# Optimization experiments

Hardware: AMD Instinct MI355X
Metric: run time of the kernel (lower is better)

The kernel has to match this reference:

```python
import jax, jax.numpy as jnp
import numpy as np

N_NODES = 100000
NEG_SLOPE = 0.2


def gat_conv(x, edge_index, W, a_src, a_dst, bias):
    """PyG GATConv, heads=1, concat, add_self_loops=True."""
    N = x.shape[0]
    loop = jnp.arange(N, dtype=edge_index.dtype)
    src = jnp.concatenate([edge_index[0], loop])  # message sources j
    dst = jnp.concatenate([edge_index[1], loop])  # message targets i
    h = x @ W                                      # [N, out]
    asrc = h @ a_src                               # [N]
    adst = h @ a_dst                               # [N]
    e = jax.nn.leaky_relu(asrc[src] + adst[dst], NEG_SLOPE)   # [E+N]
    m = jax.ops.segment_max(e, dst, num_segments=N)           # per-dst max
    w = jnp.exp(e - jax.lax.stop_gradient(m)[dst])
    denom = jax.ops.segment_sum(w, dst, num_segments=N)
    alpha = w / denom[dst]                                     # softmax per dst
    out = jax.ops.segment_sum(alpha[:, None] * h[src], dst, num_segments=N)
    return out + bias


def setup_inputs() -> dict:
    key = jax.random.key(0)
    ks = jax.random.split(key, 16)
    N, E, D = N_NODES, 3200000, 128
    x = jax.random.normal(ks[0], (N, D), dtype=jnp.float32)
    edge_index = jax.random.randint(ks[1], (2, E), 0, N, dtype=jnp.int64)
    def glorot(k, shape):
        fan = sum(shape)
        return jax.random.uniform(k, shape, jnp.float32, -1.0, 1.0) * np.sqrt(6.0 / fan)
    return {
        "x": x,
        "edge_index": edge_index,
        "W1": glorot(ks[2], (D, 16)),
        "a1_src": glorot(ks[3], (16,)),
        "a1_dst": glorot(ks[4], (16,)),
        "b1": jnp.zeros((16,), jnp.float32),
        "W2": glorot(ks[5], (16, 10)),
        "a2_src": glorot(ks[6], (10,)),
        "a2_dst": glorot(ks[7], (10,)),
        "b2": jnp.zeros((10,), jnp.float32),
        "Wl1": glorot(ks[8], (10, 10)),
        "bl1": jnp.zeros((10,), jnp.float32),
        "Wl2": glorot(ks[9], (10, 1)),
        "bl2": jnp.zeros((1,), jnp.float32),
    }


def reference(x, edge_index, W1, a1_src, a1_dst, b1, W2, a2_src, a2_dst, b2,
              Wl1, bl1, Wl2, bl2):
    h = gat_conv(x, edge_index, W1, a1_src, a1_dst, b1)
    h = jax.nn.relu(h)
    h = gat_conv(h, edge_index, W2, a2_src, a2_dst, b2)
    h = h @ Wl1 + bl1
    h = jax.nn.relu(h)
    return h @ Wl2 + bl2  # [N, 1]
```

## Files before the change

kernel.cpp:

```cpp
#include <hip/hip_runtime.h>
#include <hip/hip_fp16.h>


#define NEG 0.2f
#define FSH 8
#define BNODES 256
#define NSBMAX 512
#define CAP 9216
#define TILE 8192
#define PES 18

__device__ __forceinline__ float lrelu(float x) { return x > 0.0f ? x : NEG * x; }

__device__ __forceinline__ unsigned fenc(float f) {
    unsigned u = __float_as_uint(f);
    return (u & 0x80000000u) ? ~u : (u | 0x80000000u);
}
__device__ __forceinline__ float fdec(unsigned e) {
    return (e & 0x80000000u) ? __uint_as_float(e & 0x7FFFFFFFu) : __uint_as_float(~e);
}

__device__ __forceinline__ float4 ldh4(const __half* h, size_t off) {
    uint2 u = *(const uint2*)(h + off);
    __half2 a = *(__half2*)&u.x, b = *(__half2*)&u.y;
    float2 fa = __half22float2(a), fb = __half22float2(b);
    return make_float4(fa.x, fa.y, fb.x, fb.y);
}

__global__ __launch_bounds__(256) void k_init(unsigned* g, int* chist, int NSB) {
    int i = blockIdx.x * 256 + threadIdx.x;
    if (i < NSB) chist[i] = 0;
    if (i < 2) g[i] = 0u;
}

__global__ __launch_bounds__(256) void k_gemm1(
    const float* __restrict__ x, const float* __restrict__ W1,
    const float* __restrict__ a1s, const float* __restrict__ a1d,
    __half* __restrict__ h1, float* __restrict__ s1, float* __restrict__ d1,
    unsigned* __restrict__ gmax, int N)
{
    __shared__ float sW[128 * 16];
    __shared__ float sx[64 * 132];
    __shared__ float wm[4];
    int tid = threadIdx.x;
    for (int i = tid; i < 2048; i += 256) sW[i] = W1[i];
    int node0 = blockIdx.x * 64;
    for (int i = tid; i < 64 * 32; i += 256) {
        int row = i >> 5, c4 = i & 31;
        int n = node0 + row;
        float4 v = make_float4(0.f, 0.f, 0.f, 0.f);
        if (n < N) v = ((const float4*)x)[(size_t)n * 32 + c4];
        *(float4*)&sx[row * 132 + c4 * 4] = v;
    }
    __syncthreads();

    int node = node0 + (tid >> 2);
    int grp  = tid & 3;
    const float* xr = &sx[(tid >> 2) * 132];
    float4 acc = make_float4(0.f, 0.f, 0.f, 0.f);
#pragma unroll 8
    for (int j = 0; j < 128; ++j) {
        float xv = xr[j];
        float4 w = *(const float4*)&sW[j * 16 + grp * 4];
        acc.x += xv * w.x; acc.y += xv * w.y; acc.z += xv * w.z; acc.w += xv * w.w;
    }
    float4 as = ((const float4*)a1s)[grp];
    float4 ad = ((const float4*)a1d)[grp];
    float sv = acc.x * as.x + acc.y * as.y + acc.z * as.z + acc.w * as.w;
    float dv = acc.x * ad.x + acc.y * ad.y + acc.z * ad.z + acc.w * ad.w;
    sv += __shfl_xor(sv, 1); sv += __shfl_xor(sv, 2);
    dv += __shfl_xor(dv, 1); dv += __shfl_xor(dv, 2);
    if (node < N) {
        __half2 p0 = __floats2half2_rn(acc.x, acc.y);
        __half2 p1 = __floats2half2_rn(acc.z, acc.w);
        uint2 u; u.x = *(unsigned*)&p0; u.y = *(unsigned*)&p1;
        *(uint2*)&h1[(size_t)node * 16 + grp * 4] = u;
        if (grp == 0) { s1[node] = sv; d1[node] = dv; }
    }
    float m = (node < N) ? sv : -3.4e38f;
#pragma unroll
    for (int off = 32; off >= 1; off >>= 1) m = fmaxf(m, __shfl_xor(m, off));
    if ((tid & 63) == 0) wm[tid >> 6] = m;
    __syncthreads();
    if (tid == 0) {
        float b = fmaxf(fmaxf(wm[0], wm[1]), fmaxf(wm[2], wm[3]));
        atomicMax(gmax, fenc(b));
    }
}

__global__ __launch_bounds__(256) void k_chist(const int* __restrict__ edst,
                                               int* __restrict__ chist, int E, int NSB) {
    __shared__ int lc[NSBMAX];
    int tid = threadIdx.x;
    for (int i = tid; i < NSB; i += 256) lc[i] = 0;
    __syncthreads();
    int stride = gridDim.x * 256;
    for (int e = blockIdx.x * 256 + tid; e < E; e += stride)
        atomicAdd(&lc[edst[e] >> FSH], 1);
    __syncthreads();
    for (int i = tid; i < NSB; i += 256) { int v = lc[i]; if (v) atomicAdd(&chist[i], v); }
}

__global__ __launch_bounds__(512) void k_cboffs(const int* __restrict__ chist,
                                                int* __restrict__ cboffs, int* __restrict__ ccur,
                                                int NSB, int E) {
    __shared__ int wsum[8];
    int tid = threadIdx.x;
    int c = (tid < NSB) ? chist[tid] : 0;
    int pfx = c;
#pragma unroll
    for (int off = 1; off < 64; off <<= 1) {
        int t = __shfl_up(pfx, off, 64);
        if ((tid & 63) >= off) pfx += t;
    }
    if ((tid & 63) == 63) wsum[tid >> 6] = pfx;
    __syncthreads();
    int carry = 0;
    for (int w = 0; w < (tid >> 6); ++w) carry += wsum[w];
    pfx += carry;
    if (tid < NSB) { cboffs[tid] = pfx - c; ccur[tid * 16] = pfx - c; }
    if (tid == 0) cboffs[NSB] = E;
}

__global__ __launch_bounds__(512) void k_csplit(
    const int* __restrict__ esrc, const int* __restrict__ edst,
    int* __restrict__ ccur, unsigned* __restrict__ pairs, int E, int NSB)
{
    __shared__ unsigned lsrt[TILE];
    __shared__ int lhist[NSBMAX];
    __shared__ int lofs[NSBMAX + 1];
    __shared__ int gbase[NSBMAX];
    __shared__ int wsum[8];
    int tid = threadIdx.x;
    int base = blockIdx.x * TILE;
    int tcnt = min(TILE, E - base);
    for (int i = tid; i < NSB; i += 512) lhist[i] = 0;
    __syncthreads();
    for (int i = tid; i < tcnt; i += 512)
        atomicAdd(&lhist[edst[base + i] >> FSH], 1);
    __syncthreads();
    int c = (tid < NSB) ? lhist[tid] : 0;
    int pfx = c;
#pragma unroll
    for (int off = 1; off < 64; off <<= 1) {
        int t = __shfl_up(pfx, off, 64);
        if ((tid & 63) >= off) pfx += t;
    }
    if ((tid & 63) == 63) wsum[tid >> 6] = pfx;
    __syncthreads();
    int carry = 0;
    for (int w = 0; w < (tid >> 6); ++w) carry += wsum[w];
    pfx += carry;
    if (tid < NSB) {
        lofs[tid + 1] = pfx;
        gbase[tid] = c ? atomicAdd(&ccur[tid * 16], c) : 0;
        lhist[tid] = pfx - c;
    }
    if (tid == 0) lofs[0] = 0;
    __syncthreads();
    for (int i = tid; i < tcnt; i += 512) {
        int e = base + i;
        int d = edst[e], s = esrc[e];
        int pos = atomicAdd(&lhist[d >> FSH], 1);
        lsrt[pos] = ((unsigned)(d & (BNODES - 1)) << 17) | (unsigned)s;
    }
    __syncthreads();
    for (int i = tid; i < tcnt; i += 512) {
        int lo = 0, hi = NSB - 1;
        while (lo < hi) { int mid = (lo + hi + 1) >> 1; if (lofs[mid] <= i) lo = mid; else hi = mid - 1; }
        pairs[gbase[lo] + (i - lofs[lo])] = lsrt[i];
    }
}

__global__ __launch_bounds__(512) void k_agg1(
    const int* __restrict__ boffs, const unsigned* __restrict__ pairs,
    const float* __restrict__ s1, const float* __restrict__ d1, const __half* __restrict__ h1,
    const float* __restrict__ b1, const float* __restrict__ W2,
    const float* __restrict__ a2s, const float* __restrict__ a2d,
    __half* __restrict__ h2, float* __restrict__ s2, float* __restrict__ d2,
    const unsigned* __restrict__ gmax1p, unsigned* __restrict__ gmax2, int N)
{
    __shared__ unsigned srt[CAP];
    __shared__ float accs[BNODES * 17];
    __shared__ int lcnt[BNODES];
    __shared__ int lofs[BNODES + 1];
    __shared__ float dds[BNODES], mbs[BNODES];
    __shared__ float sW[160], sb[16], sas[16], sad[16];
    __shared__ int wsum[8];
    __shared__ float wm[8];

    int tid = threadIdx.x;
    int fb = blockIdx.x;
    if (tid < 160) sW[tid] = W2[tid];
    if (tid < 16) {
        sb[tid]  = b1[tid];
        sas[tid] = (tid < 10) ? a2s[tid] : 0.f;
        sad[tid] = (tid < 10) ? a2d[tid] : 0.f;
    }
    int node0 = fb << FSH;
    float g0 = fdec(*gmax1p);
    if (tid < BNODES) {
        int n = node0 + tid;
        float dd = (n < N) ? d1[n] : 0.f;
        dds[tid] = dd; mbs[tid] = lrelu(g0 + dd);
        lcnt[tid] = 0;
    }
    __syncthreads();

    int jbeg = boffs[fb], jend = boffs[fb + 1];
    int cnt = jend - jbeg;

    unsigned pe[PES];
#pragma unroll
    for (int u = 0; u < PES; ++u) {
        int i = tid + u * 512;
        bool ok = (i < cnt);
        pe[u] = ok ? pairs[jbeg + i] : 0u;
        if (ok) atomicAdd(&lcnt[(pe[u] >> 17) & (BNODES - 1)], 1);
    }
    __syncthreads();
    int c = (tid < BNODES) ? lcnt[tid] : 0;
    int pfx = c;
#pragma unroll
    for (int off = 1; off < 64; off <<= 1) {
        int t = __shfl_up(pfx, off, 64);
        if ((tid & 63) >= off) pfx += t;
    }
    if ((tid & 63) == 63) wsum[tid >> 6] = pfx;
    __syncthreads();
    int carry = 0;
    for (int w = 0; w < (tid >> 6); ++w) carry += wsum[w];
    pfx += carry;
    if (tid < BNODES) { lofs[tid + 1] = pfx; lcnt[tid] = pfx - c; }
    if (tid == 0) lofs[0] = 0;
    __syncthreads();
    int total = lofs[BNODES];

    int gg = tid >> 2, q = tid & 3;
    float4 accv[2]; float den[2];
#pragma unroll
    for (int qq = 0; qq < 2; ++qq) {
        int nl = gg * 2 + qq, n = node0 + nl;
        if (n < N) {
            float w = __expf(lrelu(s1[n] + dds[nl]) - mbs[nl]);
            float4 hv = ldh4(h1, (size_t)n * 16 + 4 * q);
            accv[qq] = make_float4(w * hv.x, w * hv.y, w * hv.z, w * hv.w);
            den[qq] = w;
        } else { accv[qq] = make_float4(0.f, 0.f, 0.f, 0.f); den[qq] = 0.f; }
    }

    if (total <= CAP && cnt <= CAP) {
#pragma unroll
        for (int u = 0; u < PES; ++u) {
            int i = tid + u * 512;
            if (i < cnt) {
                unsigned p = pe[u];
                int pos = atomicAdd(&lcnt[(p >> 17) & (BNODES - 1)], 1);
                srt[pos] = p & 0x1FFFF;
            }
        }
        __syncthreads();
#pragma unroll
        for (int qq = 0; qq < 2; ++qq) {
            int nl = gg * 2 + qq;
            float dd = dds[nl], mb = mbs[nl];
            int j = lofs[nl], j1 = lofs[nl + 1];
            float4 a = accv[qq]; float dn = den[qq];
            for (; j + 4 <= j1; j += 4) {
                int e0 = srt[j], e1 = srt[j + 1], e2 = srt[j + 2], e3 = srt[j + 3];
                float v0 = s1[e0], v1 = s1[e1], v2 = s1[e2], v3 = s1[e3];
                float4 H0 = ldh4(h1, (size_t)e0 * 16 + 4 * q);
                float4 H1 = ldh4(h1, (size_t)e1 * 16 + 4 * q);
                float4 H2 = ldh4(h1, (size_t)e2 * 16 + 4 * q);
                float4 H3 = ldh4(h1, (size_t)e3 * 16 + 4 * q);
                float w0 = __expf(lrelu(v0 + dd) - mb), w1 = __expf(lrelu(v1 + dd) - mb);
                float w2 = __expf(lrelu(v2 + dd) - mb), w3 = __expf(lrelu(v3 + dd) - mb);
                a.x += w0 * H0.x + w1 * H1.x + w2 * H2.x + w3 * H3.x;
                a.y += w0 * H0.y + w1 * H1.y + w2 * H2.y + w3 * H3.y;
                a.z += w0 * H0.z + w1 * H1.z + w2 * H2.z + w3 * H3.z;
                a.w += w0 * H0.w + w1 * H1.w + w2 * H2.w + w3 * H3.w;
                dn += (w0 + w1) + (w2 + w3);
            }
            for (; j < j1; ++j) {
                int e0 = srt[j];
                float w0 = __expf(lrelu(s1[e0] + dd) - mb);
                float4 H0 = ldh4(h1, (size_t)e0 * 16 + 4 * q);
                a.x += w0 * H0.x; a.y += w0 * H0.y; a.z += w0 * H0.z; a.w += w0 * H0.w;
                dn += w0;
            }
            accv[qq] = a; den[qq] = dn;
        }
        __syncthreads();
    } else {
        for (int i = tid; i < BNODES * 17; i += 512) accs[i] = 0.f;
        __syncthreads();
        for (int i = tid; i < cnt; i += 512) {
            unsigned p = pairs[jbeg + i];
            int src = p & 0x1FFFF, nl = (p >> 17) & (BNODES - 1);
            float w = __expf(lrelu(s1[src] + dds[nl]) - mbs[nl]);
            float4 H = ldh4(h1, (size_t)src * 16 + 4 * q);
            atomicAdd(&accs[nl * 17 + 4 * q + 0], w * H.x);
            atomicAdd(&accs[nl * 17 + 4 * q + 1], w * H.y);
            atomicAdd(&accs[nl * 17 + 4 * q + 2], w * H.z);
            atomicAdd(&accs[nl * 17 + 4 * q + 3], w * H.w);
            if (q == 0) atomicAdd(&accs[nl * 17 + 16], w);
        }
        __syncthreads();
#pragma unroll
        for (int qq = 0; qq < 2; ++qq) {
            int nl = gg * 2 + qq;
            accv[qq].x += accs[nl * 17 + 4 * q + 0];
            accv[qq].y += accs[nl * 17 + 4 * q + 1];
            accv[qq].z += accs[nl * 17 + 4 * q + 2];
            accv[qq].w += accs[nl * 17 + 4 * q + 3];
            den[qq] += accs[nl * 17 + 16];
        }
        __syncthreads();
    }

#pragma unroll
    for (int qq = 0; qq < 2; ++qq) {
        int nl = gg * 2 + qq;
        accs[nl * 17 + 4 * q + 0] = accv[qq].x;
        accs[nl * 17 + 4 * q + 1] = accv[qq].y;
        accs[nl * 17 + 4 * q + 2] = accv[qq].z;
        accs[nl * 17 + 4 * q + 3] = accv[qq].w;
        if (q == 0) accs[nl * 17 + 16] = den[qq];
    }
    __syncthreads();

    int g = tid >> 4, k = tid & 15;
    float sval = -3.4e38f;
#pragma unroll
    for (int qq = 0; qq < 8; ++qq) {
        int nl = g * 8 + qq, n = node0 + nl;
        if (n >= N) continue;
        float inv = 1.f / accs[nl * 17 + 16];
        float o = fmaxf(accs[nl * 17 + k] * inv + sb[k], 0.f);
        float hh = 0.f;
#pragma unroll
        for (int kk = 0; kk < 16; ++kk) {
            float ov = __shfl(o, kk, 16);
            if (k < 10) hh += ov * sW[kk * 10 + k];
        }
        if (k >= 10) hh = 0.f;
        float ts = hh * sas[k];
        float td = hh * sad[k];
#pragma unroll
        for (int off = 1; off < 16; off <<= 1) {
            ts += __shfl_xor(ts, off, 16);
            td += __shfl_xor(td, off, 16);
        }
        h2[(size_t)n * 16 + k] = __float2half_rn(hh);
        if (k == 0) { s2[n] = ts; d2[n] = td; }
        sval = fmaxf(sval, ts);
    }
    float m = sval;
#pragma unroll
    for (int off = 32; off >= 1; off >>= 1) m = fmaxf(m, __shfl_xor(m, off));
    if ((tid & 63) == 0) wm[tid >> 6] = m;
    __syncthreads();
    if (tid == 0) {
        float b = wm[0];
#pragma unroll
        for (int i = 1; i < 8; ++i) b = fmaxf(b, wm[i]);
        atomicMax(gmax2, fenc(b));
    }
}

__global__ __launch_bounds__(512) void k_agg2(
    const int* __restrict__ boffs, const unsigned* __restrict__ pairs,
    const float* __restrict__ s2, const float* __restrict__ d2, const __half* __restrict__ h2,
    const float* __restrict__ b2, const float* __restrict__ Wl1, const float* __restrict__ bl1,
    const float* __restrict__ Wl2, const float* __restrict__ bl2,
    const unsigned* __restrict__ gmax2p, float* __restrict__ out, int N)
{
    __shared__ unsigned srt[CAP];
    __shared__ float accs[BNODES * 17];
    __shared__ int lcnt[BNODES];
    __shared__ int lofs[BNODES + 1];
    __shared__ float dds[BNODES], mbs[BNODES];
    __shared__ float sW1[100], sb1[16], sW2[16], sb2g[16];
    __shared__ float sbl2;
    __shared__ int wsum[8];

    int tid = threadIdx.x;
    int fb = blockIdx.x;
    if (tid < 100) sW1[tid] = Wl1[tid];
    if (tid < 16) {
        sb1[tid]  = (tid < 10) ? bl1[tid] : 0.f;
        sW2[tid]  = (tid < 10) ? Wl2[tid] : 0.f;
        sb2g[tid] = (tid < 10) ? b2[tid]  : 0.f;
    }
    if (tid == 0) sbl2 = bl2[0];
    int node0 = fb << FSH;
    float g0 = fdec(*gmax2p);
    if (tid < BNODES) {
        int n = node0 + tid;
        float dd = (n < N) ? d2[n] : 0.f;
        dds[tid] = dd; mbs[tid] = lrelu(g0 + dd);
        lcnt[tid] = 0;
    }
    __syncthreads();

    int jbeg = boffs[fb], jend = boffs[fb + 1];
    int cnt = jend - jbeg;

    unsigned pe[PES];
#pragma unroll
    for (int u = 0; u < PES; ++u) {
        int i = tid + u * 512;
        bool ok = (i < cnt);
        pe[u] = ok ? pairs[jbeg + i] : 0u;
        if (ok) atomicAdd(&lcnt[(pe[u] >> 17) & (BNODES - 1)], 1);
    }
    __syncthreads();
    int c = (tid < BNODES) ? lcnt[tid] : 0;
    int pfx = c;
#pragma unroll
    for (int off = 1; off < 64; off <<= 1) {
        int t = __shfl_up(pfx, off, 64);
        if ((tid & 63) >= off) pfx += t;
    }
    if ((tid & 63) == 63) wsum[tid >> 6] = pfx;
    __syncthreads();
    int carry = 0;
    for (int w = 0; w < (tid >> 6); ++w) carry += wsum[w];
    pfx += carry;
    if (tid < BNODES) { lofs[tid + 1] = pfx; lcnt[tid] = pfx - c; }
    if (tid == 0) lofs[0] = 0;
    __syncthreads();
    int total = lofs[BNODES];

    int gg = tid >> 2, q = tid & 3;
    float4 accv[2]; float den[2];
#pragma unroll
    for (int qq = 0; qq < 2; ++qq) {
        int nl = gg * 2 + qq, n = node0 + nl;
        if (n < N) {
            float w = __expf(lrelu(s2[n] + dds[nl]) - mbs[nl]);
            float4 hv = ldh4(h2, (size_t)n * 16 + 4 * q);
            accv[qq] = make_float4(w * hv.x, w * hv.y, w * hv.z, w * hv.w);
            den[qq] = w;
        } else { accv[qq] = make_float4(0.f, 0.f, 0.f, 0.f); den[qq] = 0.f; }
    }

    if (total <= CAP && cnt <= CAP) {
#pragma unroll
        for (int u = 0; u < PES; ++u) {
            int i = tid + u * 512;
            if (i < cnt) {
                unsigned p = pe[u];
                int pos = atomicAdd(&lcnt[(p >> 17) & (BNODES - 1)], 1);
                srt[pos] = p & 0x1FFFF;
            }
        }
        __syncthreads();
#pragma unroll
        for (int qq = 0; qq < 2; ++qq) {
            int nl = gg * 2 + qq;
            float dd = dds[nl], mb = mbs[nl];
            int j = lofs[nl], j1 = lofs[nl + 1];
            float4 a = accv[qq]; float dn = den[qq];
            for (; j + 4 <= j1; j += 4) {
                int e0 = srt[j], e1 = srt[j + 1], e2 = srt[j + 2], e3 = srt[j + 3];
                float v0 = s2[e0], v1 = s2[e1], v2 = s2[e2], v3 = s2[e3];
                float4 H0 = ldh4(h2, (size_t)e0 * 16 + 4 * q);
                float4 H1 = ldh4(h2, (size_t)e1 * 16 + 4 * q);
                float4 H2 = ldh4(h2, (size_t)e2 * 16 + 4 * q);
                float4 H3 = ldh4(h2, (size_t)e3 * 16 + 4 * q);
                float w0 = __expf(lrelu(v0 + dd) - mb), w1 = __expf(lrelu(v1 + dd) - mb);
                float w2 = __expf(lrelu(v2 + dd) - mb), w3 = __expf(lrelu(v3 + dd) - mb);
                a.x += w0 * H0.x + w1 * H1.x + w2 * H2.x + w3 * H3.x;
                a.y += w0 * H0.y + w1 * H1.y + w2 * H2.y + w3 * H3.y;
                a.z += w0 * H0.z + w1 * H1.z + w2 * H2.z + w3 * H3.z;
                a.w += w0 * H0.w + w1 * H1.w + w2 * H2.w + w3 * H3.w;
                dn += (w0 + w1) + (w2 + w3);
            }
            for (; j < j1; ++j) {
                int e0 = srt[j];
                float w0 = __expf(lrelu(s2[e0] + dd) - mb);
                float4 H0 = ldh4(h2, (size_t)e0 * 16 + 4 * q);
                a.x += w0 * H0.x; a.y += w0 * H0.y; a.z += w0 * H0.z; a.w += w0 * H0.w;
                dn += w0;
            }
            accv[qq] = a; den[qq] = dn;
        }
        __syncthreads();
    } else {
        for (int i = tid; i < BNODES * 17; i += 512) accs[i] = 0.f;
        __syncthreads();
        for (int i = tid; i < cnt; i += 512) {
            unsigned p = pairs[jbeg + i];
            int src = p & 0x1FFFF, nl = (p >> 17) & (BNODES - 1);
            float w = __expf(lrelu(s2[src] + dds[nl]) - mbs[nl]);
            float4 H = ldh4(h2, (size_t)src * 16 + 4 * q);
            atomicAdd(&accs[nl * 17 + 4 * q + 0], w * H.x);
            atomicAdd(&accs[nl * 17 + 4 * q + 1], w * H.y);
            atomicAdd(&accs[nl * 17 + 4 * q + 2], w * H.z);
            atomicAdd(&accs[nl * 17 + 4 * q + 3], w * H.w);
            if (q == 0) atomicAdd(&accs[nl * 17 + 16], w);
        }
        __syncthreads();
#pragma unroll
        for (int qq = 0; qq < 2; ++qq) {
            int nl = gg * 2 + qq;
            accv[qq].x += accs[nl * 17 + 4 * q + 0];
            accv[qq].y += accs[nl * 17 + 4 * q + 1];
            accv[qq].z += accs[nl * 17 + 4 * q + 2];
            accv[qq].w += accs[nl * 17 + 4 * q + 3];
            den[qq] += accs[nl * 17 + 16];
        }
        __syncthreads();
    }

#pragma unroll
    for (int qq = 0; qq < 2; ++qq) {
        int nl = gg * 2 + qq;
        accs[nl * 17 + 4 * q + 0] = accv[qq].x;
        accs[nl * 17 + 4 * q + 1] = accv[qq].y;
        accs[nl * 17 + 4 * q + 2] = accv[qq].z;
        accs[nl * 17 + 4 * q + 3] = accv[qq].w;
        if (q == 0) accs[nl * 17 + 16] = den[qq];
    }
    __syncthreads();

    int g = tid >> 4, k = tid & 15;
    bool fk = k < 10;
#pragma unroll
    for (int qq = 0; qq < 8; ++qq) {
        int nl = g * 8 + qq, n = node0 + nl;
        if (n >= N) continue;
        float inv = 1.f / accs[nl * 17 + 16];
        float o = fk ? accs[nl * 17 + k] * inv + sb2g[k] : 0.f;
        float v = sb1[k];
#pragma unroll
        for (int kk = 0; kk < 10; ++kk) {
            float ov = __shfl(o, kk, 16);
            if (fk) v += ov * sW1[kk * 10 + k];
        }
        float t = fmaxf(v, 0.f);
        float cc = t * sW2[k];
#pragma unroll
        for (int off = 1; off < 16; off <<= 1) cc += __shfl_xor(cc, off, 16);
        if (k == 0) out[n] = cc + sbl2;
    }
}

extern "C" void kernel_launch(void* const* d_in, const int* in_sizes, int n_in,
                              void* d_out, int out_size, void* d_ws, size_t ws_size,
                              hipStream_t stream)
{
    const float* x   = (const float*)d_in[0];
    const int*   ei  = (const int*)  d_in[1];
    const float* W1  = (const float*)d_in[2];
    const float* a1s = (const float*)d_in[3];
    const float* a1d = (const float*)d_in[4];
    const float* b1  = (const float*)d_in[5];
    const float* W2  = (const float*)d_in[6];
    const float* a2s = (const float*)d_in[7];
    const float* a2d = (const float*)d_in[8];
    const float* b2  = (const float*)d_in[9];
    const float* Wl1 = (const float*)d_in[10];
    const float* bl1 = (const float*)d_in[11];
    const float* Wl2 = (const float*)d_in[12];
    const float* bl2 = (const float*)d_in[13];

    int N = in_sizes[0] / 128;
    int E = in_sizes[1] / 2;
    const int* ei_src = ei;
    const int* ei_dst = ei + E;
    int NSB = (N + BNODES - 1) >> FSH;

    size_t Np = ((size_t)N + 3) & ~(size_t)3;
    size_t need_bytes = (16 + Np * 20) * 4 + ((size_t)NSB * 18 + 1) * 4 + (size_t)E * 4;
    if (ws_size < need_bytes) return;

    float*    ws    = (float*)d_ws;
    unsigned* gmax1 = (unsigned*)d_ws;
    unsigned* gmax2 = gmax1 + 1;
    __half* h1 = (__half*)(ws + 16);
    float* s1 = ws + 16 + Np * 8;
    float* d1 = s1 + Np;
    __half* h2 = (__half*)(d1 + Np);
    float* s2 = (float*)(h2) + Np * 8;
    float* d2 = s2 + Np;
    int* chist  = (int*)(d2 + Np);
    int* cboffs = chist + NSB;
    int* ccur   = cboffs + NSB + 1;
    unsigned* pairs = (unsigned*)(ccur + (size_t)NSB * 16);

    hipLaunchKernelGGL(k_init, dim3((NSB + 255) / 256), dim3(256), 0, stream, gmax1, chist, NSB);
    hipLaunchKernelGGL(k_gemm1, dim3((N + 63) / 64), dim3(256), 0, stream,
                       x, W1, a1s, a1d, h1, s1, d1, gmax1, N);
    hipLaunchKernelGGL(k_chist, dim3(256), dim3(256), 0, stream, ei_dst, chist, E, NSB);
    hipLaunchKernelGGL(k_cboffs, dim3(1), dim3(512), 0, stream, chist, cboffs, ccur, NSB, E);
    hipLaunchKernelGGL(k_csplit, dim3((E + TILE - 1) / TILE), dim3(512), 0, stream,
                       ei_src, ei_dst, ccur, pairs, E, NSB);
    hipLaunchKernelGGL(k_agg1, dim3(NSB), dim3(512), 0, stream,
                       cboffs, pairs, s1, d1, h1, b1, W2, a2s, a2d, h2, s2, d2,
                       gmax1, gmax2, N);
    hipLaunchKernelGGL(k_agg2, dim3(NSB), dim3(512), 0, stream,
                       cboffs, pairs, s2, d2, h2, b2, Wl1, bl1, Wl2, bl2,
                       gmax2, (float*)d_out, N);
}
```

Measured before the change: 297.0 us.

## Halve nodes per aggregation block and spread edge-weight exp across lanes

Shrinks the destination-node bucket from 256 to 128 nodes, which doubles the number of buckets and aggregation blocks and halves the per-block LDS staging buffer. Each quad of lanes now owns one node instead of two, so the per-thread loops over two nodes are removed. In the 4-edge unrolled loop each lane computes one exp weight and shares it with the others through quad shuffles, instead of every lane computing all four. The scan kernels now handle two buckets per thread to cover up to 1024 buckets, at the cost of more global-atomic bucket traffic in the split and smaller blocks.

```diff
diff --git a/kernel.cpp b/kernel.cpp
--- a/kernel.cpp
+++ b/kernel.cpp
@@ -3,12 +3,12 @@
 
 
 #define NEG 0.2f
-#define FSH 8
-#define BNODES 256
-#define NSBMAX 512
-#define CAP 9216
+#define FSH 7
+#define BNODES 128
+#define NSBMAX 1024
+#define CAP 4608
 #define TILE 8192
-#define PES 18
+#define PES 9
 
 __device__ __forceinline__ float lrelu(float x) { return x > 0.0f ? x : NEG * x; }
 
@@ -106,8 +106,10 @@
                                                 int NSB, int E) {
     __shared__ int wsum[8];
     int tid = threadIdx.x;
-    int c = (tid < NSB) ? chist[tid] : 0;
-    int pfx = c;
+    int i0 = 2 * tid, i1 = i0 + 1;
+    int a = (i0 < NSB) ? chist[i0] : 0;
+    int b = (i1 < NSB) ? chist[i1] : 0;
+    int s = a + b, pfx = s;
 #pragma unroll
     for (int off = 1; off < 64; off <<= 1) {
         int t = __shfl_up(pfx, off, 64);
@@ -117,8 +119,9 @@
     __syncthreads();
     int carry = 0;
     for (int w = 0; w < (tid >> 6); ++w) carry += wsum[w];
-    pfx += carry;
-    if (tid < NSB) { cboffs[tid] = pfx - c; ccur[tid * 16] = pfx - c; }
+    int excl = pfx + carry - s;
+    if (i0 < NSB) { cboffs[i0] = excl;     ccur[i0 * 16] = excl; }
+    if (i1 < NSB) { cboffs[i1] = excl + a; ccur[i1 * 16] = excl + a; }
     if (tid == 0) cboffs[NSB] = E;
 }
 
@@ -128,7 +131,7 @@
 {
     __shared__ unsigned lsrt[TILE];
     __shared__ int lhist[NSBMAX];
-    __shared__ int lofs[NSBMAX + 1];
+    __shared__ int lofs[NSBMAX];
     __shared__ int gbase[NSBMAX];
     __shared__ int wsum[8];
     int tid = threadIdx.x;
@@ -139,8 +142,10 @@
     for (int i = tid; i < tcnt; i += 512)
         atomicAdd(&lhist[edst[base + i] >> FSH], 1);
     __syncthreads();
-    int c = (tid < NSB) ? lhist[tid] : 0;
-    int pfx = c;
+    int i0 = 2 * tid, i1 = i0 + 1;
+    int a = (i0 < NSB) ? lhist[i0] : 0;
+    int b = (i1 < NSB) ? lhist[i1] : 0;
+    int s = a + b, pfx = s;
 #pragma unroll
     for (int off = 1; off < 64; off <<= 1) {
         int t = __shfl_up(pfx, off, 64);
@@ -150,19 +155,24 @@
     __syncthreads();
     int carry = 0;
     for (int w = 0; w < (tid >> 6); ++w) carry += wsum[w];
-    pfx += carry;
-    if (tid < NSB) {
-        lofs[tid + 1] = pfx;
-        gbase[tid] = c ? atomicAdd(&ccur[tid * 16], c) : 0;
-        lhist[tid] = pfx - c;
-    }
-    if (tid == 0) lofs[0] = 0;
+    int excl = pfx + carry - s;
+    if (i0 < NSB) {
+        lofs[i0] = excl;
+        gbase[i0] = a ? atomicAdd(&ccur[i0 * 16], a) : 0;
+    }
+    if (i1 < NSB) {
+        lofs[i1] = excl + a;
+        gbase[i1] = b ? atomicAdd(&ccur[i1 * 16], b) : 0;
+    }
+    __syncthreads();
+    if (i0 < NSB) lhist[i0] = lofs[i0];
+    if (i1 < NSB) lhist[i1] = lofs[i1];
     __syncthreads();
     for (int i = tid; i < tcnt; i += 512) {
         int e = base + i;
-        int d = edst[e], s = esrc[e];
+        int d = edst[e], srcv = esrc[e];
         int pos = atomicAdd(&lhist[d >> FSH], 1);
-        lsrt[pos] = ((unsigned)(d & (BNODES - 1)) << 17) | (unsigned)s;
+        lsrt[pos] = ((unsigned)(d & (BNODES - 1)) << 17) | (unsigned)srcv;
     }
     __syncthreads();
     for (int i = tid; i < tcnt; i += 512) {
@@ -237,17 +247,14 @@
     int total = lofs[BNODES];
 
     int gg = tid >> 2, q = tid & 3;
-    float4 accv[2]; float den[2];
-#pragma unroll
-    for (int qq = 0; qq < 2; ++qq) {
-        int nl = gg * 2 + qq, n = node0 + nl;
-        if (n < N) {
-            float w = __expf(lrelu(s1[n] + dds[nl]) - mbs[nl]);
-            float4 hv = ldh4(h1, (size_t)n * 16 + 4 * q);
-            accv[qq] = make_float4(w * hv.x, w * hv.y, w * hv.z, w * hv.w);
-            den[qq] = w;
-        } else { accv[qq] = make_float4(0.f, 0.f, 0.f, 0.f); den[qq] = 0.f; }
-    }
+    int n = node0 + gg;
+    float4 accv; float den;
+    if (n < N) {
+        float w = __expf(lrelu(s1[n] + dds[gg]) - mbs[gg]);
+        float4 hv = ldh4(h1, (size_t)n * 16 + 4 * q);
+        accv = make_float4(w * hv.x, w * hv.y, w * hv.z, w * hv.w);
+        den = w;
+    } else { accv = make_float4(0.f, 0.f, 0.f, 0.f); den = 0.f; }
 
     if (total <= CAP && cnt <= CAP) {
 #pragma unroll
@@ -260,35 +267,33 @@
             }
         }
         __syncthreads();
-#pragma unroll
-        for (int qq = 0; qq < 2; ++qq) {
-            int nl = gg * 2 + qq;
-            float dd = dds[nl], mb = mbs[nl];
-            int j = lofs[nl], j1 = lofs[nl + 1];
-            float4 a = accv[qq]; float dn = den[qq];
+        {
+            float dd = dds[gg], mb = mbs[gg];
+            int j = lofs[gg], j1 = lofs[gg + 1];
             for (; j + 4 <= j1; j += 4) {
                 int e0 = srt[j], e1 = srt[j + 1], e2 = srt[j + 2], e3 = srt[j + 3];
-                float v0 = s1[e0], v1 = s1[e1], v2 = s1[e2], v3 = s1[e3];
                 float4 H0 = ldh4(h1, (size_t)e0 * 16 + 4 * q);
                 float4 H1 = ldh4(h1, (size_t)e1 * 16 + 4 * q);
                 float4 H2 = ldh4(h1, (size_t)e2 * 16 + 4 * q);
                 float4 H3 = ldh4(h1, (size_t)e3 * 16 + 4 * q);
-                float w0 = __expf(lrelu(v0 + dd) - mb), w1 = __expf(lrelu(v1 + dd) - mb);
-                float w2 = __expf(lrelu(v2 + dd) - mb), w3 = __expf(lrelu(v3 + dd) - mb);
-                a.x += w0 * H0.x + w1 * H1.x + w2 * H2.x + w3 * H3.x;
-                a.y += w0 * H0.y + w1 * H1.y + w2 * H2.y + w3 * H3.y;
-                a.z += w0 * H0.z + w1 * H1.z + w2 * H2.z + w3 * H3.z;
-                a.w += w0 * H0.w + w1 * H1.w + w2 * H2.w + w3 * H3.w;
-                dn += (w0 + w1) + (w2 + w3);
+                int eq = srt[j + q];
+                float wq = __expf(lrelu(s1[eq] + dd) - mb);
+                float w0 = __shfl(wq, 0, 4), w1 = __shfl(wq, 1, 4);
+                float w2 = __shfl(wq, 2, 4), w3 = __shfl(wq, 3, 4);
+                accv.x += w0 * H0.x + w1 * H1.x + w2 * H2.x + w3 * H3.x;
+                accv.y += w0 * H0.y + w1 * H1.y + w2 * H2.y + w3 * H3.y;
+                accv.z += w0 * H0.z + w1 * H1.z + w2 * H2.z + w3 * H3.z;
+                accv.w += w0 * H0.w + w1 * H1.w + w2 * H2.w + w3 * H3.w;
+                den += (w0 + w1) + (w2 + w3);
             }
             for (; j < j1; ++j) {
                 int e0 = srt[j];
                 float w0 = __expf(lrelu(s1[e0] + dd) - mb);
                 float4 H0 = ldh4(h1, (size_t)e0 * 16 + 4 * q);
-                a.x += w0 * H0.x; a.y += w0 * H0.y; a.z += w0 * H0.z; a.w += w0 * H0.w;
-                dn += w0;
+                accv.x += w0 * H0.x; accv.y += w0 * H0.y;
+                accv.z += w0 * H0.z; accv.w += w0 * H0.w;
+                den += w0;
             }
-            accv[qq] = a; den[qq] = dn;
         }
         __syncthreads();
     } else {
@@ -306,35 +311,27 @@
             if (q == 0) atomicAdd(&accs[nl * 17 + 16], w);
         }
         __syncthreads();
-#pragma unroll
-        for (int qq = 0; qq < 2; ++qq) {
-            int nl = gg * 2 + qq;
-            accv[qq].x += accs[nl * 17 + 4 * q + 0];
-            accv[qq].y += accs[nl * 17 + 4 * q + 1];
-            accv[qq].z += accs[nl * 17 + 4 * q + 2];
-            accv[qq].w += accs[nl * 17 + 4 * q + 3];
-            den[qq] += accs[nl * 17 + 16];
-        }
-        __syncthreads();
-    }
-
-#pragma unroll
-    for (int qq = 0; qq < 2; ++qq) {
-        int nl = gg * 2 + qq;
-        accs[nl * 17 + 4 * q + 0] = accv[qq].x;
-        accs[nl * 17 + 4 * q + 1] = accv[qq].y;
-        accs[nl * 17 + 4 * q + 2] = accv[qq].z;
-        accs[nl * 17 + 4 * q + 3] = accv[qq].w;
-        if (q == 0) accs[nl * 17 + 16] = den[qq];
-    }
+        accv.x += accs[gg * 17 + 4 * q + 0];
+        accv.y += accs[gg * 17 + 4 * q + 1];
+        accv.z += accs[gg * 17 + 4 * q + 2];
+        accv.w += accs[gg * 17 + 4 * q + 3];
+        den += accs[gg * 17 + 16];
+        __syncthreads();
+    }
+
+    accs[gg * 17 + 4 * q + 0] = accv.x;
+    accs[gg * 17 + 4 * q + 1] = accv.y;
+    accs[gg * 17 + 4 * q + 2] = accv.z;
+    accs[gg * 17 + 4 * q + 3] = accv.w;
+    if (q == 0) accs[gg * 17 + 16] = den;
     __syncthreads();
 
     int g = tid >> 4, k = tid & 15;
     float sval = -3.4e38f;
 #pragma unroll
-    for (int qq = 0; qq < 8; ++qq) {
-        int nl = g * 8 + qq, n = node0 + nl;
-        if (n >= N) continue;
+    for (int qq = 0; qq < 4; ++qq) {
+        int nl = g * 4 + qq, nn = node0 + nl;
+        if (nn >= N) continue;
         float inv = 1.f / accs[nl * 17 + 16];
         float o = fmaxf(accs[nl * 17 + k] * inv + sb[k], 0.f);
         float hh = 0.f;
@@ -351,8 +348,8 @@
             ts += __shfl_xor(ts, off, 16);
             td += __shfl_xor(td, off, 16);
         }
-        h2[(size_t)n * 16 + k] = __float2half_rn(hh);
-        if (k == 0) { s2[n] = ts; d2[n] = td; }
+        h2[(size_t)nn * 16 + k] = __float2half_rn(hh);
+        if (k == 0) { s2[nn] = ts; d2[nn] = td; }
         sval = fmaxf(sval, ts);
     }
     float m = sval;
@@ -361,10 +358,10 @@
     if ((tid & 63) == 0) wm[tid >> 6] = m;
     __syncthreads();
     if (tid == 0) {
-        float b = wm[0];
-#pragma unroll
-        for (int i = 1; i < 8; ++i) b = fmaxf(b, wm[i]);
-        atomicMax(gmax2, fenc(b));
+        float bmx = wm[0];
+#pragma unroll
+        for (int i = 1; i < 8; ++i) bmx = fmaxf(bmx, wm[i]);
+        atomicMax(gmax2, fenc(bmx));
     }
 }
 
@@ -433,17 +430,14 @@
     int total = lofs[BNODES];
 
     int gg = tid >> 2, q = tid & 3;
-    float4 accv[2]; float den[2];
-#pragma unroll
-    for (int qq = 0; qq < 2; ++qq) {
-        int nl = gg * 2 + qq, n = node0 + nl;
-        if (n < N) {
-            float w = __expf(lrelu(s2[n] + dds[nl]) - mbs[nl]);
-            float4 hv = ldh4(h2, (size_t)n * 16 + 4 * q);
-            accv[qq] = make_float4(w * hv.x, w * hv.y, w * hv.z, w * hv.w);
-            den[qq] = w;
-        } else { accv[qq] = make_float4(0.f, 0.f, 0.f, 0.f); den[qq] = 0.f; }
-    }
+    int n = node0 + gg;
+    float4 accv; float den;
+    if (n < N) {
+        float w = __expf(lrelu(s2[n] + dds[gg]) - mbs[gg]);
+        float4 hv = ldh4(h2, (size_t)n * 16 + 4 * q);
+        accv = make_float4(w * hv.x, w * hv.y, w * hv.z, w * hv.w);
+        den = w;
+    } else { accv = make_float4(0.f, 0.f, 0.f, 0.f); den = 0.f; }
 
     if (total <= CAP && cnt <= CAP) {
 #pragma unroll
@@ -456,35 +450,33 @@
             }
         }
         __syncthreads();
-#pragma unroll
-        for (int qq = 0; qq < 2; ++qq) {
-            int nl = gg * 2 + qq;
-            float dd = dds[nl], mb = mbs[nl];
-            int j = lofs[nl], j1 = lofs[nl + 1];
-            float4 a = accv[qq]; float dn = den[qq];
+        {
+            float dd = dds[gg], mb = mbs[gg];
+            int j = lofs[gg], j1 = lofs[gg + 1];
             for (; j + 4 <= j1; j += 4) {
                 int e0 = srt[j], e1 = srt[j + 1], e2 = srt[j + 2], e3 = srt[j + 3];
-                float v0 = s2[e0], v1 = s2[e1], v2 = s2[e2], v3 = s2[e3];
                 float4 H0 = ldh4(h2, (size_t)e0 * 16 + 4 * q);
                 float4 H1 = ldh4(h2, (size_t)e1 * 16 + 4 * q);
                 float4 H2 = ldh4(h2, (size_t)e2 * 16 + 4 * q);
                 float4 H3 = ldh4(h2, (size_t)e3 * 16 + 4 * q);
-                float w0 = __expf(lrelu(v0 + dd) - mb), w1 = __expf(lrelu(v1 + dd) - mb);
-                float w2 = __expf(lrelu(v2 + dd) - mb), w3 = __expf(lrelu(v3 + dd) - mb);
-                a.x += w0 * H0.x + w1 * H1.x + w2 * H2.x + w3 * H3.x;
-                a.y += w0 * H0.y + w1 * H1.y + w2 * H2.y + w3 * H3.y;
-                a.z += w0 * H0.z + w1 * H1.z + w2 * H2.z + w3 * H3.z;
-                a.w += w0 * H0.w + w1 * H1.w + w2 * H2.w + w3 * H3.w;
-                dn += (w0 + w1) + (w2 + w3);
+                int eq = srt[j + q];
+                float wq = __expf(lrelu(s2[eq] + dd) - mb);
+                float w0 = __shfl(wq, 0, 4), w1 = __shfl(wq, 1, 4);
+                float w2 = __shfl(wq, 2, 4), w3 = __shfl(wq, 3, 4);
+                accv.x += w0 * H0.x + w1 * H1.x + w2 * H2.x + w3 * H3.x;
+                accv.y += w0 * H0.y + w1 * H1.y + w2 * H2.y + w3 * H3.y;
+                accv.z += w0 * H0.z + w1 * H1.z + w2 * H2.z + w3 * H3.z;
+                accv.w += w0 * H0.w + w1 * H1.w + w2 * H2.w + w3 * H3.w;
+                den += (w0 + w1) + (w2 + w3);
             }
             for (; j < j1; ++j) {
                 int e0 = srt[j];
                 float w0 = __expf(lrelu(s2[e0] + dd) - mb);
                 float4 H0 = ldh4(h2, (size_t)e0 * 16 + 4 * q);
-                a.x += w0 * H0.x; a.y += w0 * H0.y; a.z += w0 * H0.z; a.w += w0 * H0.w;
-                dn += w0;
+                accv.x += w0 * H0.x; accv.y += w0 * H0.y;
+                accv.z += w0 * H0.z; accv.w += w0 * H0.w;
+                den += w0;
             }
-            accv[qq] = a; den[qq] = dn;
         }
         __syncthreads();
     } else {
@@ -502,35 +494,27 @@
             if (q == 0) atomicAdd(&accs[nl * 17 + 16], w);
         }
         __syncthreads();
-#pragma unroll
-        for (int qq = 0; qq < 2; ++qq) {
-            int nl = gg * 2 + qq;
-            accv[qq].x += accs[nl * 17 + 4 * q + 0];
-            accv[qq].y += accs[nl * 17 + 4 * q + 1];
-            accv[qq].z += accs[nl * 17 + 4 * q + 2];
-            accv[qq].w += accs[nl * 17 + 4 * q + 3];
-            den[qq] += accs[nl * 17 + 16];
-        }
-        __syncthreads();
-    }
-
-#pragma unroll
-    for (int qq = 0; qq < 2; ++qq) {
-        int nl = gg * 2 + qq;
-        accs[nl * 17 + 4 * q + 0] = accv[qq].x;
-        accs[nl * 17 + 4 * q + 1] = accv[qq].y;
-        accs[nl * 17 + 4 * q + 2] = accv[qq].z;
-        accs[nl * 17 + 4 * q + 3] = accv[qq].w;
-        if (q == 0) accs[nl * 17 + 16] = den[qq];
-    }
+        accv.x += accs[gg * 17 + 4 * q + 0];
+        accv.y += accs[gg * 17 + 4 * q + 1];
+        accv.z += accs[gg * 17 + 4 * q + 2];
+        accv.w += accs[gg * 17 + 4 * q + 3];
+        den += accs[gg * 17 + 16];
+        __syncthreads();
+    }
+
+    accs[gg * 17 + 4 * q + 0] = accv.x;
+    accs[gg * 17 + 4 * q + 1] = accv.y;
+    accs[gg * 17 + 4 * q + 2] = accv.z;
+    accs[gg * 17 + 4 * q + 3] = accv.w;
+    if (q == 0) accs[gg * 17 + 16] = den;
     __syncthreads();
 
     int g = tid >> 4, k = tid & 15;
     bool fk = k < 10;
 #pragma unroll
-    for (int qq = 0; qq < 8; ++qq) {
-        int nl = g * 8 + qq, n = node0 + nl;
-        if (n >= N) continue;
+    for (int qq = 0; qq < 4; ++qq) {
+        int nl = g * 4 + qq, nn = node0 + nl;
+        if (nn >= N) continue;
         float inv = 1.f / accs[nl * 17 + 16];
         float o = fk ? accs[nl * 17 + k] * inv + sb2g[k] : 0.f;
         float v = sb1[k];
@@ -543,7 +527,7 @@
         float cc = t * sW2[k];
 #pragma unroll
         for (int off = 1; off < 16; off <<= 1) cc += __shfl_xor(cc, off, 16);
-        if (k == 0) out[n] = cc + sbl2;
+        if (k == 0) out[nn] = cc + sbl2;
     }
 }
 
```

Result: no change. 292.7 us (-1.4%).
